# Kernel optimization log

Hardware: AMD Instinct MI355X
Metric: run time of the kernel (lower is better)

The kernel has to match this reference:

```python
import jax, jax.numpy as jnp
import numpy as np

CAUSAL = True
SOFTMAX_SCALE = 0.125
K_DIFF = 192
MASK_FILL = -1000000.0


def setup_inputs() -> dict:
    key = jax.random.key(0)
    ks = jax.random.split(key, 5)
    shape = (1, 8, 192, 64)  # [batch, n_heads, seq, head_dim]
    return {
        "q": jax.random.normal(ks[0], shape, dtype=jnp.float32),
        "k1": jax.random.normal(ks[1], shape, dtype=jnp.float32),
        "k2": jax.random.normal(ks[2], shape, dtype=jnp.float32),
        "v1": jax.random.normal(ks[3], shape, dtype=jnp.float32),
        "v2": jax.random.normal(ks[4], shape, dtype=jnp.float32),
    }


def reference(q, k1, k2, v1, v2):
    b, n, S, h = q.shape
    # Third-order (trittention) scores.
    score_qk = jnp.einsum("bnth,bnqh->bntq", k2, q)   # [b,n,t,q]
    score_kk = jnp.einsum("bnsh,bnth->bnst", k1, k2)  # [b,n,s,t]
    # score[b,n,s,t,q] = score_kk[b,n,s,t] + score_qk[b,n,t,q]
    score = score_kk[..., None] + score_qk[:, :, None, :, :]
    if CAUSAL:
        # Torch mask (dims named t,s,q over score dims s,t,q):
        # masked where s_score > t_score, t_score > q_score, or t_score - s_score > k_diff
        s_i = jnp.arange(S)[:, None, None]
        t_i = jnp.arange(S)[None, :, None]
        q_i = jnp.arange(S)[None, None, :]
        mask = (s_i > t_i) | (t_i > q_i) | (t_i - s_i > K_DIFF)
        score = jnp.where(mask, MASK_FILL, score)
    pre_softmax_attn_score = score  # [b,n,s,t,q]
    # Rearrange 'b n s t q -> b n q (s t)' and scale.
    flat = jnp.transpose(score, (0, 1, 4, 2, 3)).reshape(b, n, S, S * S) * SOFTMAX_SCALE
    M0 = jnp.max(flat, axis=-1)                       # [b,n,q]
    p = jax.nn.softmax(flat, axis=-1)                  # standard softmax (no +0.01)
    L = jnp.sum(jnp.exp(flat - M0[..., None]), axis=-1) + 0.01
    M = M0 + jnp.log(L)                                # non-standard LSE with +0.01
    # SiLU-gated value combination: v[b,n,s,t,h] = silu(v1[s]) * v2[t]
    v_gated = jax.nn.silu(v1)[:, :, :, None, :] * v2[:, :, None, :, :]
    v_flat = jnp.transpose(v_gated, (0, 1, 4, 2, 3)).reshape(b, n, h, S * S)
    z = jnp.einsum("bnql,bnhl->bnqh", p, v_flat)
    return (z, pre_softmax_attn_score, v_gated, M)
```

## Files before the change

kernel.cpp:

```cpp
#include <hip/hip_runtime.h>
#include <math.h>

#define S 192
#define H 64
#define NH 8
#define SC 0.125f
#define FILLV (-1000000.0f)

__device__ __forceinline__ float wave_max(float v) {
#pragma unroll
  for (int m = 32; m; m >>= 1) v = fmaxf(v, __shfl_xor(v, m));
  return v;
}
__device__ __forceinline__ float wave_sum(float v) {
#pragma unroll
  for (int m = 32; m; m >>= 1) v += __shfl_xor(v, m);
  return v;
}

__global__ void prep_kernel(const float* __restrict__ q, const float* __restrict__ k1,
                            const float* __restrict__ k2, const float* __restrict__ v1,
                            float* __restrict__ kk, float* __restrict__ qk,
                            float* __restrict__ sv1) {
  int b = blockIdx.x;
  if (b < 576) {
    bool is_kk = (b < 288);
    int bb = is_kk ? b : b - 288;
    int n = bb / 36;
    int rem = bb % 36;
    int rt = (rem / 6) * 32;
    int ct = (rem % 6) * 32;
    const float* Abase = (is_kk ? k1 : k2) + n * S * H;
    const float* Bbase = (is_kk ? k2 : q) + n * S * H;
    float* out = (is_kk ? kk : qk) + n * S * S;

    __shared__ float As[32][65];
    __shared__ float Bs[32][65];
    int tid = threadIdx.x;
    for (int i = tid; i < 32 * 64; i += 256) {
      int r = i >> 6, h = i & 63;
      As[r][h] = Abase[(rt + r) * H + h];
      Bs[r][h] = Bbase[(ct + r) * H + h];
    }
    __syncthreads();
    int r0 = (tid / 16) * 2, c0 = (tid % 16) * 2;
    float a00 = 0.f, a01 = 0.f, a10 = 0.f, a11 = 0.f;
#pragma unroll
    for (int h = 0; h < 64; ++h) {
      float x0 = As[r0][h], x1 = As[r0 + 1][h];
      float y0 = Bs[c0][h], y1 = Bs[c0 + 1][h];
      a00 += x0 * y0; a01 += x0 * y1; a10 += x1 * y0; a11 += x1 * y1;
    }
    out[(rt + r0) * S + ct + c0]         = a00;
    out[(rt + r0) * S + ct + c0 + 1]     = a01;
    out[(rt + r0 + 1) * S + ct + c0]     = a10;
    out[(rt + r0 + 1) * S + ct + c0 + 1] = a11;
  } else {
    int i = (b - 576) * 256 + threadIdx.x;
    const float4* v4 = (const float4*)v1;
    float4 x = v4[i];
    float4 y;
    y.x = x.x / (1.f + expf(-x.x));
    y.y = x.y / (1.f + expf(-x.y));
    y.z = x.z / (1.f + expf(-x.z));
    y.w = x.w / (1.f + expf(-x.w));
    ((float4*)sv1)[i] = y;
  }
}

__global__ void stats_kernel(const float* __restrict__ kk, const float* __restrict__ sv1,
                             float* __restrict__ mt, float* __restrict__ St,
                             float* __restrict__ Aw) {
  int n = blockIdx.x / S, t = blockIdx.x % S;
  int lane = threadIdx.x;
  __shared__ float w[S];
  const float* kkc = kk + n * S * S + t;

  float lm = -3.4e38f;
  for (int s = lane; s <= t; s += 64) lm = fmaxf(lm, SC * kkc[s * S]);
  float m = wave_max(lm);

  float ls = 0.f;
  for (int s = lane; s <= t; s += 64) {
    float e = expf(SC * kkc[s * S] - m);
    w[s] = e;
    ls += e;
  }
  float Ssum = wave_sum(ls);
  if (lane == 0) { mt[n * S + t] = m; St[n * S + t] = Ssum; }
  __syncthreads();

  const float* sh = sv1 + n * S * H + lane;
  float acc = 0.f;
  for (int s = 0; s <= t; ++s) acc += w[s] * sh[s * H];
  Aw[(n * S + t) * H + lane] = acc;
}

__global__ void out_kernel(const float* __restrict__ qk, const float* __restrict__ v2,
                           const float* __restrict__ mt, const float* __restrict__ St,
                           const float* __restrict__ Aw,
                           float* __restrict__ z, float* __restrict__ Mout) {
  int n = blockIdx.x / S, qq = blockIdx.x % S;
  int lane = threadIdx.x;
  __shared__ float e[S];
  const float* qkc = qk + n * S * S + qq;

  float lm = -3.4e38f;
  for (int t = lane; t <= qq; t += 64) lm = fmaxf(lm, SC * qkc[t * S] + mt[n * S + t]);
  float M0 = wave_max(lm);

  float ls = 0.f;
  for (int t = lane; t <= qq; t += 64) {
    float ev = expf(SC * qkc[t * S] + mt[n * S + t] - M0);
    e[t] = ev;
    ls += ev * St[n * S + t];
  }
  float D = wave_sum(ls);
  if (lane == 0) Mout[n * S + qq] = M0 + logf(D + 0.01f);
  __syncthreads();

  const float* vh = v2 + n * S * H + lane;
  const float* Ah = Aw + n * S * H + lane;
  float acc = 0.f;
  for (int t = 0; t <= qq; ++t) acc += e[t] * vh[t * H] * Ah[t * H];
  z[(n * S + qq) * H + lane] = acc / D;
}

__global__ void score_kernel(const float* __restrict__ kk, const float* __restrict__ qk,
                             float* __restrict__ score) {
  int n = blockIdx.x / S, s = blockIdx.x % S;
  const float* kkr = kk + (n * S + s) * S;
  const float4* qk4 = (const float4*)(qk + n * S * S);
  float4* out4 = (float4*)(score + (size_t)(n * S + s) * S * S);
  const float4 fill = make_float4(FILLV, FILLV, FILLV, FILLV);

  for (int i = threadIdx.x; i < S * 48; i += 256) {
    int t = i / 48, j = i - t * 48;
    float4 v;
    if (t < s) {
      v = fill;
    } else {
      float kv = kkr[t];
      float4 qv = qk4[t * 48 + j];
      int q0 = 4 * j;
      v.x = (t > q0)     ? FILLV : kv + qv.x;
      v.y = (t > q0 + 1) ? FILLV : kv + qv.y;
      v.z = (t > q0 + 2) ? FILLV : kv + qv.z;
      v.w = (t > q0 + 3) ? FILLV : kv + qv.w;
    }
    out4[i] = v;
  }
}

__global__ void vg_kernel(const float* __restrict__ sv1, const float* __restrict__ v2,
                          float* __restrict__ vg) {
  int n = blockIdx.x / S, s = blockIdx.x % S;
  const float4* a4 = (const float4*)(sv1 + (n * S + s) * H);
  const float4* b4 = (const float4*)(v2 + n * S * H);
  float4* out4 = (float4*)(vg + (size_t)(n * S + s) * S * H);

  for (int i = threadIdx.x; i < S * 16; i += 256) {
    int t = i >> 4, j = i & 15;
    float4 a = a4[j];
    float4 b = b4[t * 16 + j];
    out4[i] = make_float4(a.x * b.x, a.y * b.y, a.z * b.z, a.w * b.w);
  }
}

extern "C" void kernel_launch(void* const* d_in, const int* in_sizes, int n_in,
                              void* d_out, int out_size, void* d_ws, size_t ws_size,
                              hipStream_t stream) {
  const float* q  = (const float*)d_in[0];
  const float* k1 = (const float*)d_in[1];
  const float* k2 = (const float*)d_in[2];
  const float* v1 = (const float*)d_in[3];
  const float* v2 = (const float*)d_in[4];
  float* out = (float*)d_out;

  float* z     = out;
  float* score = out + 98304;
  float* vg    = out + 98304 + 56623104;
  float* Mout  = out + 98304 + 56623104 + 18874368;

  float* ws  = (float*)d_ws;
  float* kk  = ws;
  float* qk  = ws + 294912;
  float* sv1 = ws + 589824;
  float* mt  = ws + 688128;
  float* St  = ws + 689664;
  float* Aw  = ws + 691200;

  prep_kernel<<<dim3(672), dim3(256), 0, stream>>>(q, k1, k2, v1, kk, qk, sv1);
  stats_kernel<<<dim3(NH * S), dim3(64), 0, stream>>>(kk, sv1, mt, St, Aw);
  out_kernel<<<dim3(NH * S), dim3(64), 0, stream>>>(qk, v2, mt, St, Aw, z, Mout);
  score_kernel<<<dim3(NH * S), dim3(256), 0, stream>>>(kk, qk, score);
  vg_kernel<<<dim3(NH * S), dim3(256), 0, stream>>>(sv1, v2, vg);
}
```

Before: 390.8 us.

## Use nontemporal stores for large outputs and widen stats/out kernels to four waves

The score and gated-value writes, which make up most of the runtime (about 300 MB of output), now use nontemporal stores so streaming data bypasses cache retention. The score kernel's block size doubles to 512 threads. The stats and out kernels go from one wave to four waves per block, with block-level reductions through shared memory and partial accumulators summed at the end. This shortens the serial per-row loops, at the cost of extra syncthreads.

```diff
diff --git a/kernel.cpp b/kernel.cpp
--- a/kernel.cpp
+++ b/kernel.cpp
@@ -6,6 +6,8 @@
 #define NH 8
 #define SC 0.125f
 #define FILLV (-1000000.0f)
+
+typedef float floatx4 __attribute__((ext_vector_type(4)));
 
 __device__ __forceinline__ float wave_max(float v) {
 #pragma unroll
@@ -68,77 +70,103 @@
   }
 }
 
-__global__ void stats_kernel(const float* __restrict__ kk, const float* __restrict__ sv1,
-                             float* __restrict__ mt, float* __restrict__ St,
-                             float* __restrict__ Aw) {
+__global__ __launch_bounds__(256) void stats_kernel(
+    const float* __restrict__ kk, const float* __restrict__ sv1,
+    float* __restrict__ mt, float* __restrict__ St, float* __restrict__ Aw) {
   int n = blockIdx.x / S, t = blockIdx.x % S;
-  int lane = threadIdx.x;
+  int tid = threadIdx.x, wv = tid >> 6, lane = tid & 63;
   __shared__ float w[S];
+  __shared__ float red[4];
+  __shared__ float part[4][H];
   const float* kkc = kk + n * S * S + t;
 
   float lm = -3.4e38f;
-  for (int s = lane; s <= t; s += 64) lm = fmaxf(lm, SC * kkc[s * S]);
-  float m = wave_max(lm);
+  for (int s = tid; s <= t; s += 256) lm = fmaxf(lm, SC * kkc[s * S]);
+  lm = wave_max(lm);
+  if (lane == 0) red[wv] = lm;
+  __syncthreads();
+  float m = fmaxf(fmaxf(red[0], red[1]), fmaxf(red[2], red[3]));
 
   float ls = 0.f;
-  for (int s = lane; s <= t; s += 64) {
+  for (int s = tid; s <= t; s += 256) {
     float e = expf(SC * kkc[s * S] - m);
     w[s] = e;
     ls += e;
   }
-  float Ssum = wave_sum(ls);
-  if (lane == 0) { mt[n * S + t] = m; St[n * S + t] = Ssum; }
-  __syncthreads();
+  ls = wave_sum(ls);
+  __syncthreads();
+  if (lane == 0) red[wv] = ls;
+  __syncthreads();
+  float Ssum = red[0] + red[1] + red[2] + red[3];
+  if (tid == 0) { mt[n * S + t] = m; St[n * S + t] = Ssum; }
 
   const float* sh = sv1 + n * S * H + lane;
   float acc = 0.f;
-  for (int s = 0; s <= t; ++s) acc += w[s] * sh[s * H];
-  Aw[(n * S + t) * H + lane] = acc;
-}
-
-__global__ void out_kernel(const float* __restrict__ qk, const float* __restrict__ v2,
-                           const float* __restrict__ mt, const float* __restrict__ St,
-                           const float* __restrict__ Aw,
-                           float* __restrict__ z, float* __restrict__ Mout) {
+  for (int s = wv; s <= t; s += 4) acc += w[s] * sh[s * H];
+  part[wv][lane] = acc;
+  __syncthreads();
+  if (wv == 0)
+    Aw[(n * S + t) * H + lane] = part[0][lane] + part[1][lane] + part[2][lane] + part[3][lane];
+}
+
+__global__ __launch_bounds__(256) void out_kernel(
+    const float* __restrict__ qk, const float* __restrict__ v2,
+    const float* __restrict__ mt, const float* __restrict__ St,
+    const float* __restrict__ Aw,
+    float* __restrict__ z, float* __restrict__ Mout) {
   int n = blockIdx.x / S, qq = blockIdx.x % S;
-  int lane = threadIdx.x;
+  int tid = threadIdx.x, wv = tid >> 6, lane = tid & 63;
   __shared__ float e[S];
+  __shared__ float red[4];
+  __shared__ float part[4][H];
   const float* qkc = qk + n * S * S + qq;
+  const float* mtp = mt + n * S;
+  const float* Stp = St + n * S;
 
   float lm = -3.4e38f;
-  for (int t = lane; t <= qq; t += 64) lm = fmaxf(lm, SC * qkc[t * S] + mt[n * S + t]);
-  float M0 = wave_max(lm);
+  for (int t = tid; t <= qq; t += 256) lm = fmaxf(lm, SC * qkc[t * S] + mtp[t]);
+  lm = wave_max(lm);
+  if (lane == 0) red[wv] = lm;
+  __syncthreads();
+  float M0 = fmaxf(fmaxf(red[0], red[1]), fmaxf(red[2], red[3]));
 
   float ls = 0.f;
-  for (int t = lane; t <= qq; t += 64) {
-    float ev = expf(SC * qkc[t * S] + mt[n * S + t] - M0);
+  for (int t = tid; t <= qq; t += 256) {
+    float ev = expf(SC * qkc[t * S] + mtp[t] - M0);
     e[t] = ev;
-    ls += ev * St[n * S + t];
-  }
-  float D = wave_sum(ls);
-  if (lane == 0) Mout[n * S + qq] = M0 + logf(D + 0.01f);
-  __syncthreads();
+    ls += ev * Stp[t];
+  }
+  ls = wave_sum(ls);
+  __syncthreads();
+  if (lane == 0) red[wv] = ls;
+  __syncthreads();
+  float D = red[0] + red[1] + red[2] + red[3];
+  if (tid == 0) Mout[n * S + qq] = M0 + logf(D + 0.01f);
 
   const float* vh = v2 + n * S * H + lane;
   const float* Ah = Aw + n * S * H + lane;
   float acc = 0.f;
-  for (int t = 0; t <= qq; ++t) acc += e[t] * vh[t * H] * Ah[t * H];
-  z[(n * S + qq) * H + lane] = acc / D;
-}
-
-__global__ void score_kernel(const float* __restrict__ kk, const float* __restrict__ qk,
-                             float* __restrict__ score) {
+  for (int t = wv; t <= qq; t += 4) acc += e[t] * vh[t * H] * Ah[t * H];
+  part[wv][lane] = acc;
+  __syncthreads();
+  if (wv == 0)
+    z[(n * S + qq) * H + lane] =
+        (part[0][lane] + part[1][lane] + part[2][lane] + part[3][lane]) / D;
+}
+
+__global__ __launch_bounds__(512) void score_kernel(
+    const float* __restrict__ kk, const float* __restrict__ qk,
+    float* __restrict__ score) {
   int n = blockIdx.x / S, s = blockIdx.x % S;
   const float* kkr = kk + (n * S + s) * S;
   const float4* qk4 = (const float4*)(qk + n * S * S);
-  float4* out4 = (float4*)(score + (size_t)(n * S + s) * S * S);
-  const float4 fill = make_float4(FILLV, FILLV, FILLV, FILLV);
-
-  for (int i = threadIdx.x; i < S * 48; i += 256) {
+  floatx4* out4 = (floatx4*)(score + (size_t)(n * S + s) * S * S);
+
+  for (int i = threadIdx.x; i < S * 48; i += 512) {
     int t = i / 48, j = i - t * 48;
-    float4 v;
+    floatx4 v;
     if (t < s) {
-      v = fill;
+      v = (floatx4){FILLV, FILLV, FILLV, FILLV};
     } else {
       float kv = kkr[t];
       float4 qv = qk4[t * 48 + j];
@@ -148,22 +176,24 @@
       v.z = (t > q0 + 2) ? FILLV : kv + qv.z;
       v.w = (t > q0 + 3) ? FILLV : kv + qv.w;
     }
-    out4[i] = v;
-  }
-}
-
-__global__ void vg_kernel(const float* __restrict__ sv1, const float* __restrict__ v2,
-                          float* __restrict__ vg) {
+    __builtin_nontemporal_store(v, &out4[i]);
+  }
+}
+
+__global__ __launch_bounds__(256) void vg_kernel(
+    const float* __restrict__ sv1, const float* __restrict__ v2,
+    float* __restrict__ vg) {
   int n = blockIdx.x / S, s = blockIdx.x % S;
   const float4* a4 = (const float4*)(sv1 + (n * S + s) * H);
   const float4* b4 = (const float4*)(v2 + n * S * H);
-  float4* out4 = (float4*)(vg + (size_t)(n * S + s) * S * H);
+  floatx4* out4 = (floatx4*)(vg + (size_t)(n * S + s) * S * H);
 
   for (int i = threadIdx.x; i < S * 16; i += 256) {
     int t = i >> 4, j = i & 15;
     float4 a = a4[j];
     float4 b = b4[t * 16 + j];
-    out4[i] = make_float4(a.x * b.x, a.y * b.y, a.z * b.z, a.w * b.w);
+    floatx4 v = (floatx4){a.x * b.x, a.y * b.y, a.z * b.z, a.w * b.w};
+    __builtin_nontemporal_store(v, &out4[i]);
   }
 }
 
@@ -191,8 +221,8 @@
   float* Aw  = ws + 691200;
 
   prep_kernel<<<dim3(672), dim3(256), 0, stream>>>(q, k1, k2, v1, kk, qk, sv1);
-  stats_kernel<<<dim3(NH * S), dim3(64), 0, stream>>>(kk, sv1, mt, St, Aw);
-  out_kernel<<<dim3(NH * S), dim3(64), 0, stream>>>(qk, v2, mt, St, Aw, z, Mout);
-  score_kernel<<<dim3(NH * S), dim3(256), 0, stream>>>(kk, qk, score);
+  stats_kernel<<<dim3(NH * S), dim3(256), 0, stream>>>(kk, sv1, mt, St, Aw);
+  out_kernel<<<dim3(NH * S), dim3(256), 0, stream>>>(qk, v2, mt, St, Aw, z, Mout);
+  score_kernel<<<dim3(NH * S), dim3(512), 0, stream>>>(kk, qk, score);
   vg_kernel<<<dim3(NH * S), dim3(256), 0, stream>>>(sv1, v2, vg);
 }
```

Measured after the change: 356.9 us. -8.7%, faster.
